# Kernel optimization log

Measured on AMD Instinct MI355X. Metric: run time of the kernel, lower is better.

Reference implementation:

```python
import jax, jax.numpy as jnp
import numpy as np

N = 50000      # nodes
E = 800000     # edges (avg degree 16)
CIN = 64       # in_channels
COUT = 128     # hidden_channels (block out_channels)
TC = 512       # time_channels = 4*hidden
H = 4          # attention heads
DH = COUT // H # head dim
G = 8          # group-norm groups
SLOPE = 0.01   # LeakyReLU default slope


def group_norm(x, w, b, groups=G, eps=1e-5):
    n, c = x.shape
    xg = x.reshape(n, groups, c // groups)
    mu = xg.mean(-1, keepdims=True)
    var = xg.var(-1, keepdims=True)
    xn = ((xg - mu) * jax.lax.rsqrt(var + eps)).reshape(n, c)
    return xn * w + b


def gcn_conv(x, W, b, row, col, ew, n):
    # GCNConv: add self loops (weight 1), symmetric normalization
    sl = jnp.arange(n)
    r = jnp.concatenate([row, sl])
    c = jnp.concatenate([col, sl])
    w2 = jnp.concatenate([ew, jnp.ones((n,), ew.dtype)])
    deg = jax.ops.segment_sum(w2, c, num_segments=n)
    dinv = jnp.where(deg > 0, jax.lax.rsqrt(deg), 0.0)
    norm = dinv[r] * w2 * dinv[c]            # [E+N]
    xw = x @ W                                # [N, Cout]
    out = jax.ops.segment_sum(norm[:, None] * xw[r], c, num_segments=n)
    return out + b


def gat_conv(x, Wa, a_src, a_dst, a_edge, ba, row, col, ew, n):
    # GAT-style attention conv; self-loop edge weight filled with max(edge_weight)
    sl = jnp.arange(n)
    fill = ew.max()
    r = jnp.concatenate([row, sl])
    c = jnp.concatenate([col, sl])
    w2 = jnp.concatenate([ew, jnp.full((n,), fill, ew.dtype)])
    h = (x @ Wa).reshape(n, H, DH)            # [N, H, DH]
    al_s = (h * a_src).sum(-1)                # [N, H]
    al_d = (h * a_dst).sum(-1)                # [N, H]
    logits = jax.nn.leaky_relu(al_s[r] + al_d[c] + a_edge * w2[:, None], 0.2)
    m = jax.ops.segment_max(logits, c, num_segments=n)
    e = jnp.exp(logits - m[c])
    s = jax.ops.segment_sum(e, c, num_segments=n)
    alpha = e / (s[c] + 1e-16)                # [E+N, H]
    out = jax.ops.segment_sum(alpha[:, :, None] * h[r], c, num_segments=n)
    return out.reshape(n, H * DH) + ba


def setup_inputs() -> dict:
    key = jax.random.key(0)
    ks = jax.random.split(key, 24)
    def w(k, shape, fan_in):
        return (jax.random.normal(k, shape, jnp.float32) / np.sqrt(fan_in)).astype(jnp.float32)
    inp = {
        "x": jax.random.normal(ks[0], (N, CIN), jnp.float32),
        "t": jax.random.normal(ks[1], (TC,), jnp.float32),
        "edge_index": jax.random.randint(ks[2], (2, E), 0, N, jnp.int32),
        "edge_weight": jax.random.uniform(ks[3], (E,), jnp.float32),
        # ResBlock norm/conv params
        "gn0_w": jnp.ones((CIN,), jnp.float32), "gn0_b": jnp.zeros((CIN,), jnp.float32),
        "W1": w(ks[4], (CIN, COUT), CIN), "b1": jnp.zeros((COUT,), jnp.float32),
        "gn1_w": jnp.ones((COUT,), jnp.float32), "gn1_b": jnp.zeros((COUT,), jnp.float32),
        "W2": w(ks[5], (COUT, COUT), COUT), "b2": jnp.zeros((COUT,), jnp.float32),
        "Wres": w(ks[6], (CIN, COUT), CIN),
        "te_w": w(ks[7], (TC, COUT), TC), "te_b": jnp.zeros((COUT,), jnp.float32),
        # AttnBlock params
        "gn2_w": jnp.ones((COUT,), jnp.float32), "gn2_b": jnp.zeros((COUT,), jnp.float32),
        "Wa": w(ks[8], (COUT, H * DH), COUT),
        "a_src": w(ks[9], (H, DH), DH), "a_dst": w(ks[10], (H, DH), DH),
        "a_edge": w(ks[11], (H,), 1), "ba": jnp.zeros((H * DH,), jnp.float32),
    }
    return inp


def reference(x, t, edge_index, edge_weight,
              gn0_w, gn0_b, W1, b1, gn1_w, gn1_b, W2, b2, Wres, te_w, te_b,
              gn2_w, gn2_b, Wa, a_src, a_dst, a_edge, ba):
    row, col = edge_index[0], edge_index[1]
    leaky = lambda z: jax.nn.leaky_relu(z, SLOPE)
    # ResBlock (n_layers=2)
    h = gcn_conv(leaky(group_norm(x, gn0_w, gn0_b)), W1, b1, row, col, edge_weight, N)
    tt = leaky(t) @ te_w + te_b               # time embed, broadcasts over nodes
    h = h + tt
    h = gcn_conv(leaky(group_norm(h, gn1_w, gn1_b)), W2, b2, row, col, edge_weight, N)
    h = h + x @ Wres                          # residual (Cin != Cout -> Linear)
    # AttnBlock (n_layers=1)
    a = leaky(group_norm(h, gn2_w, gn2_b))
    out = gat_conv(a, Wa, a_src, a_dst, a_edge, ba, row, col, edge_weight, N)
    return out
```

## Files before the change

kernel.cpp:

```cpp
#include <hip/hip_runtime.h>
#include <math.h>

#define ELLW 48
#define CH 4096
#define BCAP 8192

typedef __attribute__((ext_vector_type(8))) short frag_ab;
typedef __attribute__((ext_vector_type(4))) float frag_cd;

__device__ __forceinline__ float lk(float v, float s) { return v > 0.f ? v : v * s; }
__device__ __forceinline__ unsigned short f2b(float f) {
    unsigned u = __float_as_uint(f);
    return (unsigned short)((u + 0x7fffu + ((u >> 16) & 1u)) >> 16);
}
__device__ __forceinline__ float b2f(unsigned h) { return __uint_as_float(h << 16); }

template <int K>
__device__ __forceinline__ void repack1(const float* __restrict__ W,
                                        unsigned short* __restrict__ Wp, int i) {
    int k = i >> 7, nn = i & 127;
    int kc = k >> 5, quad = (k >> 3) & 3, j = k & 7;
    Wp[(((size_t)(kc * 4 + quad) * 128) + nn) * 8 + j] = f2b(W[i]);
}

__global__ __launch_bounds__(256) void k_bscatter(const int* __restrict__ row,
                                                  const int* __restrict__ col,
                                                  const float* __restrict__ ew,
                                                  int* __restrict__ cursor,
                                                  uint2* __restrict__ stage,
                                                  float* __restrict__ bmax,
                                                  int E, int NB, int gridE,
                                                  const float* __restrict__ t,
                                                  const float* __restrict__ te_w,
                                                  const float* __restrict__ te_b,
                                                  const float* __restrict__ b1,
                                                  float* __restrict__ tt,
                                                  const float* __restrict__ W1,
                                                  const float* __restrict__ W2,
                                                  const float* __restrict__ Wa,
                                                  const float* __restrict__ Wres,
                                                  unsigned short* W1p, unsigned short* W2p,
                                                  unsigned short* Wap, unsigned short* Wrp) {
    int tid = threadIdx.x;
    int blk = blockIdx.x;
    if (blk >= gridE) {
        if (blk == gridE) {
            if (tid < 128) {
                float s = te_b[tid] + b1[tid];
                for (int k = 0; k < 512; ++k) {
                    float tv = t[k]; tv = tv > 0.f ? tv : 0.01f * tv;
                    s = fmaf(tv, te_w[k * 128 + tid], s);
                }
                tt[tid] = s;
            }
        } else {
            int i = (blk - gridE - 1) * 256 + tid;
            if (i < 8192)        repack1<64>(W1, W1p, i);
            else if (i < 24576)  repack1<128>(W2, W2p, i - 8192);
            else if (i < 40960)  repack1<128>(Wa, Wap, i - 24576);
            else if (i < 49152)  repack1<64>(Wres, Wrp, i - 40960);
        }
        return;
    }
    __shared__ int lh[256];
    __shared__ int lbase[256];
    constexpr int PT = CH / 256;
    if (tid < NB) lh[tid] = 0;
    __syncthreads();
    int base = blk * CH;
    unsigned entry[PT]; int cc[PT]; int lpos[PT]; bool val[PT];
    float m = 0.f;
#pragma unroll
    for (int i = 0; i < PT; ++i) {
        int e = base + i * 256 + tid;
        val[i] = (e < E);
        entry[i] = 0; cc[i] = 0; lpos[i] = 0;
        if (val[i]) {
            int r = row[e], c = col[e];
            float w = ew[e];
            m = fmaxf(m, w);
            entry[i] = (unsigned)r | ((unsigned)f2b(w) << 16);
            cc[i] = c;
            lpos[i] = atomicAdd(&lh[c >> 8], 1);
        }
    }
    __syncthreads();
    if (tid < NB) lbase[tid] = lh[tid] ? atomicAdd(&cursor[tid], lh[tid]) : 0;
    __syncthreads();
#pragma unroll
    for (int i = 0; i < PT; ++i) {
        if (val[i]) {
            int b = cc[i] >> 8;
            int pos = lbase[b] + lpos[i];
            if (pos < BCAP)
                stage[(size_t)b * BCAP + pos] = make_uint2(entry[i], (unsigned)(cc[i] & 255));
        }
    }
    for (int o = 32; o; o >>= 1) m = fmaxf(m, __shfl_down(m, o, 64));
    __shared__ float sm[4];
    if ((tid & 63) == 0) sm[tid >> 6] = m;
    __syncthreads();
    if (tid == 0) bmax[blk] = fmaxf(fmaxf(sm[0], sm[1]), fmaxf(sm[2], sm[3]));
}

__global__ __launch_bounds__(256) void k_bbuild(const int* __restrict__ cursor,
                                                const uint2* __restrict__ stage,
                                                unsigned* __restrict__ ell,
                                                int* __restrict__ cnt,
                                                float* __restrict__ dinv,
                                                const float* __restrict__ bmax,
                                                float* __restrict__ fill, int n, int nbm) {
    __shared__ unsigned tile[256 * ELLW];
    __shared__ int lcnt[256];
    int tid = threadIdx.x;
    int bk = blockIdx.x;
    lcnt[tid] = 0;
    __syncthreads();
    if (bk == 0) {
        float m = 0.f;
        for (int i = tid; i < nbm; i += 256) m = fmaxf(m, bmax[i]);
        for (int o = 32; o; o >>= 1) m = fmaxf(m, __shfl_down(m, o, 64));
        __shared__ float sm[4];
        if ((tid & 63) == 0) sm[tid >> 6] = m;
        __syncthreads();
        if (tid == 0) *fill = fmaxf(fmaxf(sm[0], sm[1]), fmaxf(sm[2], sm[3]));
    }
    int bc = min(cursor[bk], BCAP);
    const uint2* sp = stage + (size_t)bk * BCAP;
    for (int i = tid; i < bc; i += 256) {
        uint2 p = sp[i];
        int c8 = p.y;
        int pos = atomicAdd(&lcnt[c8], 1);
        if (pos < ELLW) tile[c8 * ELLW + pos] = p.x;
    }
    __syncthreads();
    int node = bk * 256 + tid;
    if (node >= n) return;
    int c = min(lcnt[tid], ELLW);
    cnt[node] = c;
    float sw = 1.f;
    for (int j = 0; j < c; ++j) sw += b2f(tile[tid * ELLW + j] >> 16);
    dinv[node] = rsqrtf(sw);
    unsigned* dst = ell + (size_t)node * ELLW;
#pragma unroll
    for (int j = 0; j < ELLW / 4; ++j)
        *(uint4*)(dst + j * 4) = *(uint4*)(tile + tid * ELLW + j * 4);
}

__global__ __launch_bounds__(256) void k_mgemm1(const float* __restrict__ X,
                                                const float* __restrict__ gw,
                                                const float* __restrict__ gb,
                                                const unsigned short* __restrict__ Wp,
                                                unsigned short* __restrict__ OUTh,
                                                unsigned short* __restrict__ xh,
                                                const float* __restrict__ dinv, int n) {
    int tid = threadIdx.x;
    int wave = tid >> 6, lane = tid & 63;
    int quad = lane >> 4, l16 = lane & 15;
    int rbase = blockIdx.x * 64 + wave * 16;
    int arow = rbase + l16; if (arow >= n) arow = n - 1;
    frag_ab afrag[2];
    const float* xr = X + (size_t)arow * 64 + quad * 8;
#pragma unroll
    for (int kc = 0; kc < 2; ++kc) {
        float4 u0 = *(const float4*)(xr + kc * 32);
        float4 u1 = *(const float4*)(xr + kc * 32 + 4);
        float v[8] = {u0.x, u0.y, u0.z, u0.w, u1.x, u1.y, u1.z, u1.w};
        float s = 0.f, sq = 0.f;
#pragma unroll
        for (int j = 0; j < 8; ++j) { s += v[j]; sq = fmaf(v[j], v[j], sq); }
        float mu = s * 0.125f;
        float var = sq * 0.125f - mu * mu;
        float rstd = rsqrtf(var + 1e-5f);
        const float* wj = gw + kc * 32 + quad * 8;
        const float* bj = gb + kc * 32 + quad * 8;
        unsigned pk[4], pr[4];
#pragma unroll
        for (int j = 0; j < 8; j += 2) {
            float y0 = lk((v[j + 0] - mu) * rstd * wj[j + 0] + bj[j + 0], 0.01f);
            float y1 = lk((v[j + 1] - mu) * rstd * wj[j + 1] + bj[j + 1], 0.01f);
            pk[j / 2] = (unsigned)f2b(y0) | ((unsigned)f2b(y1) << 16);
            pr[j / 2] = (unsigned)f2b(v[j]) | ((unsigned)f2b(v[j + 1]) << 16);
        }
        afrag[kc] = *(frag_ab*)pk;
        *(uint4*)(xh + (size_t)arow * 64 + kc * 32 + quad * 8) = *(uint4*)pr;
    }
    frag_cd acc[8];
#pragma unroll
    for (int t = 0; t < 8; ++t) acc[t] = (frag_cd){0.f, 0.f, 0.f, 0.f};
#pragma unroll
    for (int kc = 0; kc < 2; ++kc) {
        const unsigned short* bp = Wp + ((size_t)(kc * 4 + quad) * 128 + l16) * 8;
#pragma unroll
        for (int t = 0; t < 8; ++t) {
            frag_ab b = *(const frag_ab*)(bp + (size_t)t * 128);
            acc[t] = __builtin_amdgcn_mfma_f32_16x16x32_bf16(afrag[kc], b, acc[t], 0, 0, 0);
        }
    }
#pragma unroll
    for (int reg = 0; reg < 4; ++reg) {
        int r = rbase + quad * 4 + reg;
        if (r >= n) continue;
        float sc = dinv[r];
#pragma unroll
        for (int t = 0; t < 8; ++t)
            OUTh[(size_t)r * 128 + t * 16 + l16] = f2b(sc * acc[t][reg]);
    }
}

__global__ __launch_bounds__(256) void k_mgemm2(const unsigned short* __restrict__ X1,
                                                const unsigned short* __restrict__ W2p,
                                                const unsigned short* __restrict__ X2,
                                                const unsigned short* __restrict__ Wrp,
                                                unsigned short* __restrict__ OUTh,
                                                float* __restrict__ C2,
                                                const float* __restrict__ bias,
                                                const float* __restrict__ dinv, int n) {
    int tid = threadIdx.x;
    int wave = tid >> 6, lane = tid & 63;
    int quad = lane >> 4, l16 = lane & 15;
    int rbase = blockIdx.x * 64 + wave * 16;
    int arow = rbase + l16; if (arow >= n) arow = n - 1;
    frag_cd acc1[8], acc2[8];
#pragma unroll
    for (int t = 0; t < 8; ++t) {
        acc1[t] = (frag_cd){0.f, 0.f, 0.f, 0.f};
        acc2[t] = (frag_cd){0.f, 0.f, 0.f, 0.f};
    }
    const unsigned short* ap1 = X1 + (size_t)arow * 128 + quad * 8;
#pragma unroll
    for (int kc = 0; kc < 4; ++kc) {
        frag_ab a = *(const frag_ab*)(ap1 + kc * 32);
        const unsigned short* bp = W2p + ((size_t)(kc * 4 + quad) * 128 + l16) * 8;
#pragma unroll
        for (int t = 0; t < 8; ++t) {
            frag_ab b = *(const frag_ab*)(bp + (size_t)t * 128);
            acc1[t] = __builtin_amdgcn_mfma_f32_16x16x32_bf16(a, b, acc1[t], 0, 0, 0);
        }
    }
    const unsigned short* ap2 = X2 + (size_t)arow * 64 + quad * 8;
#pragma unroll
    for (int kc = 0; kc < 2; ++kc) {
        frag_ab a = *(const frag_ab*)(ap2 + kc * 32);
        const unsigned short* bp = Wrp + ((size_t)(kc * 4 + quad) * 128 + l16) * 8;
#pragma unroll
        for (int t = 0; t < 8; ++t) {
            frag_ab b = *(const frag_ab*)(bp + (size_t)t * 128);
            acc2[t] = __builtin_amdgcn_mfma_f32_16x16x32_bf16(a, b, acc2[t], 0, 0, 0);
        }
    }
#pragma unroll
    for (int reg = 0; reg < 4; ++reg) {
        int r = rbase + quad * 4 + reg;
        if (r >= n) continue;
        float sc = dinv[r];
#pragma unroll
        for (int t = 0; t < 8; ++t) {
            int c = t * 16 + l16;
            size_t o = (size_t)r * 128 + c;
            OUTh[o] = f2b(sc * acc1[t][reg]);
            C2[o] = bias[c] + acc2[t][reg];
        }
    }
}

__global__ __launch_bounds__(256) void k_mgemmA(const unsigned short* __restrict__ Xh,
                                                const unsigned short* __restrict__ Wp,
                                                unsigned short* __restrict__ OUTh,
                                                const float* __restrict__ a_src,
                                                const float* __restrict__ a_dst,
                                                float* __restrict__ als,
                                                float* __restrict__ ald, int n) {
    int tid = threadIdx.x;
    int wave = tid >> 6, lane = tid & 63;
    int quad = lane >> 4, l16 = lane & 15;
    int rbase = blockIdx.x * 64 + wave * 16;
    int arow = rbase + l16; if (arow >= n) arow = n - 1;
    frag_cd acc[8];
#pragma unroll
    for (int t = 0; t < 8; ++t) acc[t] = (frag_cd){0.f, 0.f, 0.f, 0.f};
    const unsigned short* ap = Xh + (size_t)arow * 128 + quad * 8;
#pragma unroll
    for (int kc = 0; kc < 4; ++kc) {
        frag_ab a = *(const frag_ab*)(ap + kc * 32);
        const unsigned short* bp = Wp + ((size_t)(kc * 4 + quad) * 128 + l16) * 8;
#pragma unroll
        for (int t = 0; t < 8; ++t) {
            frag_ab b = *(const frag_ab*)(bp + (size_t)t * 128);
            acc[t] = __builtin_amdgcn_mfma_f32_16x16x32_bf16(a, b, acc[t], 0, 0, 0);
        }
    }
#pragma unroll
    for (int reg = 0; reg < 4; ++reg) {
        int r = rbase + quad * 4 + reg;
        if (r >= n) continue;
#pragma unroll
        for (int t = 0; t < 8; ++t)
            OUTh[(size_t)r * 128 + t * 16 + l16] = f2b(acc[t][reg]);
    }
    float ps[4][4], pd[4][4];
#pragma unroll
    for (int hd = 0; hd < 4; ++hd) {
        float slo = a_src[hd * 32 + l16], shi = a_src[hd * 32 + 16 + l16];
        float dlo = a_dst[hd * 32 + l16], dhi = a_dst[hd * 32 + 16 + l16];
#pragma unroll
        for (int reg = 0; reg < 4; ++reg) {
            ps[reg][hd] = fmaf(acc[2 * hd][reg], slo, acc[2 * hd + 1][reg] * shi);
            pd[reg][hd] = fmaf(acc[2 * hd][reg], dlo, acc[2 * hd + 1][reg] * dhi);
        }
    }
#pragma unroll
    for (int m = 1; m < 16; m <<= 1) {
#pragma unroll
        for (int reg = 0; reg < 4; ++reg)
#pragma unroll
            for (int hd = 0; hd < 4; ++hd) {
                ps[reg][hd] += __shfl_xor(ps[reg][hd], m, 64);
                pd[reg][hd] += __shfl_xor(pd[reg][hd], m, 64);
            }
    }
    if (l16 == 0) {
#pragma unroll
        for (int reg = 0; reg < 4; ++reg) {
            int r = rbase + quad * 4 + reg;
            if (r >= n) continue;
#pragma unroll
            for (int hd = 0; hd < 4; ++hd) {
                als[r * 4 + hd] = ps[reg][hd];
                ald[r * 4 + hd] = pd[reg][hd];
            }
        }
    }
}

template <int BASEVEC>
__global__ __launch_bounds__(256) void k_gather_gn(const int* __restrict__ cnt,
                                                   const unsigned* __restrict__ ell,
                                                   const float* __restrict__ dinv,
                                                   const unsigned short* __restrict__ Bh,
                                                   const float* __restrict__ basevec,
                                                   const float* __restrict__ basebuf,
                                                   const float* __restrict__ gw,
                                                   const float* __restrict__ gb,
                                                   unsigned short* __restrict__ outh, int n) {
    int gid = blockIdx.x * 256 + threadIdx.x;
    int node = gid >> 5, q = gid & 31;
    if (node >= n) return;
    int s = node * ELLW;
    int e2 = s + min(cnt[node], ELLW);
    float a0 = 0.f, a1 = 0.f, a2 = 0.f, a3 = 0.f;
    int j = s;
    for (; j + 8 <= e2; j += 8) {
        uint4 pa = *(const uint4*)(ell + j);
        uint4 pb = *(const uint4*)(ell + j + 4);
        unsigned pe[8] = {pa.x, pa.y, pa.z, pa.w, pb.x, pb.y, pb.z, pb.w};
        uint2 v[8];
#pragma unroll
        for (int k = 0; k < 8; ++k)
            v[k] = *(const uint2*)(Bh + (size_t)(pe[k] & 0xffffu) * 128 + q * 4);
#pragma unroll
        for (int k = 0; k < 8; ++k) {
            float w = b2f(pe[k] >> 16);
            a0 = fmaf(w, b2f(v[k].x & 0xffffu), a0);
            a1 = fmaf(w, b2f(v[k].x >> 16), a1);
            a2 = fmaf(w, b2f(v[k].y & 0xffffu), a2);
            a3 = fmaf(w, b2f(v[k].y >> 16), a3);
        }
    }
    if (j + 4 <= e2) {
        uint4 pa = *(const uint4*)(ell + j);
        unsigned pe[4] = {pa.x, pa.y, pa.z, pa.w};
        uint2 v[4];
#pragma unroll
        for (int k = 0; k < 4; ++k)
            v[k] = *(const uint2*)(Bh + (size_t)(pe[k] & 0xffffu) * 128 + q * 4);
#pragma unroll
        for (int k = 0; k < 4; ++k) {
            float w = b2f(pe[k] >> 16);
            a0 = fmaf(w, b2f(v[k].x & 0xffffu), a0);
            a1 = fmaf(w, b2f(v[k].x >> 16), a1);
            a2 = fmaf(w, b2f(v[k].y & 0xffffu), a2);
            a3 = fmaf(w, b2f(v[k].y >> 16), a3);
        }
        j += 4;
    }
    for (; j < e2; ++j) {
        unsigned pe = ell[j];
        float nw = b2f(pe >> 16);
        uint2 hv = *(const uint2*)(Bh + (size_t)(pe & 0xffffu) * 128 + q * 4);
        a0 = fmaf(nw, b2f(hv.x & 0xffffu), a0);
        a1 = fmaf(nw, b2f(hv.x >> 16), a1);
        a2 = fmaf(nw, b2f(hv.y & 0xffffu), a2);
        a3 = fmaf(nw, b2f(hv.y >> 16), a3);
    }
    float dc = dinv[node];
    uint2 sv = *(const uint2*)(Bh + (size_t)node * 128 + q * 4);
    a0 = dc * (a0 + b2f(sv.x & 0xffffu));
    a1 = dc * (a1 + b2f(sv.x >> 16));
    a2 = dc * (a2 + b2f(sv.y & 0xffffu));
    a3 = dc * (a3 + b2f(sv.y >> 16));
    float h0, h1, h2, h3;
    if constexpr (BASEVEC) {
        float4 bb = *(const float4*)(basevec + q * 4);
        h0 = bb.x + a0; h1 = bb.y + a1; h2 = bb.z + a2; h3 = bb.w + a3;
    } else {
        float4 bb = *(const float4*)(basebuf + (size_t)node * 128 + q * 4);
        h0 = bb.x + a0; h1 = bb.y + a1; h2 = bb.z + a2; h3 = bb.w + a3;
    }
    float sum = (h0 + h1) + (h2 + h3);
    float sq = fmaf(h0, h0, fmaf(h1, h1, fmaf(h2, h2, h3 * h3)));
    sum += __shfl_xor(sum, 1, 64); sum += __shfl_xor(sum, 2, 64);
    sq  += __shfl_xor(sq, 1, 64);  sq  += __shfl_xor(sq, 2, 64);
    float mu = sum * (1.0f / 16.0f);
    float var = sq * (1.0f / 16.0f) - mu * mu;
    float rstd = rsqrtf(var + 1e-5f);
    float4 gwv = *(const float4*)(gw + q * 4);
    float4 gbv = *(const float4*)(gb + q * 4);
    float y0 = lk((h0 - mu) * rstd * gwv.x + gbv.x, 0.01f);
    float y1 = lk((h1 - mu) * rstd * gwv.y + gbv.y, 0.01f);
    float y2 = lk((h2 - mu) * rstd * gwv.z + gbv.z, 0.01f);
    float y3 = lk((h3 - mu) * rstd * gwv.w + gbv.w, 0.01f);
    uint2 o;
    o.x = (unsigned)f2b(y0) | ((unsigned)f2b(y1) << 16);
    o.y = (unsigned)f2b(y2) | ((unsigned)f2b(y3) << 16);
    *(uint2*)(outh + (size_t)node * 128 + q * 4) = o;
}

__global__ __launch_bounds__(256) void k_gat_gather(const int* __restrict__ cnt,
                                                    const unsigned* __restrict__ ell,
                                                    const float* __restrict__ als,
                                                    const float* __restrict__ ald,
                                                    const float* __restrict__ a_edge,
                                                    const float* __restrict__ fill,
                                                    const unsigned short* __restrict__ HAh,
                                                    const float* __restrict__ ba,
                                                    float* __restrict__ out, int n) {
    int gid = blockIdx.x * 256 + threadIdx.x;
    int node = gid >> 5, q = gid & 31, hd = q >> 3;
    if (node >= n) return;
    int s = node * ELLW;
    int e2 = s + min(cnt[node], ELLW);
    float ae = a_edge[hd];
    float aldc = ald[node * 4 + hd];
    float wself = *fill;
    float pself = __expf(lk(als[node * 4 + hd] + aldc + ae * wself, 0.2f));
    float den = pself;
    uint2 hv = *(const uint2*)(HAh + (size_t)node * 128 + q * 4);
    float a0 = pself * b2f(hv.x & 0xffffu), a1 = pself * b2f(hv.x >> 16);
    float a2 = pself * b2f(hv.y & 0xffffu), a3 = pself * b2f(hv.y >> 16);
    int j = s;
    for (; j + 8 <= e2; j += 8) {
        uint4 pa = *(const uint4*)(ell + j);
        uint4 pb = *(const uint4*)(ell + j + 4);
        unsigned pe[8] = {pa.x, pa.y, pa.z, pa.w, pb.x, pb.y, pb.z, pb.w};
        float sl[8]; uint2 v[8];
#pragma unroll
        for (int k = 0; k < 8; ++k) {
            int r = pe[k] & 0xffffu;
            sl[k] = als[r * 4 + hd];
            v[k] = *(const uint2*)(HAh + (size_t)r * 128 + q * 4);
        }
#pragma unroll
        for (int k = 0; k < 8; ++k) {
            float pev = __expf(lk(sl[k] + aldc + ae * b2f(pe[k] >> 16), 0.2f));
            den += pev;
            a0 = fmaf(pev, b2f(v[k].x & 0xffffu), a0);
            a1 = fmaf(pev, b2f(v[k].x >> 16), a1);
            a2 = fmaf(pev, b2f(v[k].y & 0xffffu), a2);
            a3 = fmaf(pev, b2f(v[k].y >> 16), a3);
        }
    }
    if (j + 4 <= e2) {
        uint4 pa = *(const uint4*)(ell + j);
        unsigned pe[4] = {pa.x, pa.y, pa.z, pa.w};
        float sl[4]; uint2 v[4];
#pragma unroll
        for (int k = 0; k < 4; ++k) {
            int r = pe[k] & 0xffffu;
            sl[k] = als[r * 4 + hd];
            v[k] = *(const uint2*)(HAh + (size_t)r * 128 + q * 4);
        }
#pragma unroll
        for (int k = 0; k < 4; ++k) {
            float pev = __expf(lk(sl[k] + aldc + ae * b2f(pe[k] >> 16), 0.2f));
            den += pev;
            a0 = fmaf(pev, b2f(v[k].x & 0xffffu), a0);
            a1 = fmaf(pev, b2f(v[k].x >> 16), a1);
            a2 = fmaf(pev, b2f(v[k].y & 0xffffu), a2);
            a3 = fmaf(pev, b2f(v[k].y >> 16), a3);
        }
        j += 4;
    }
    for (; j < e2; ++j) {
        unsigned pe = ell[j];
        int r = pe & 0xffffu;
        float pev = __expf(lk(als[r * 4 + hd] + aldc + ae * b2f(pe >> 16), 0.2f));
        den += pev;
        uint2 v = *(const uint2*)(HAh + (size_t)r * 128 + q * 4);
        a0 = fmaf(pev, b2f(v.x & 0xffffu), a0);
        a1 = fmaf(pev, b2f(v.x >> 16), a1);
        a2 = fmaf(pev, b2f(v.y & 0xffffu), a2);
        a3 = fmaf(pev, b2f(v.y >> 16), a3);
    }
    float inv = 1.0f / (den + 1e-16f);
    const float* bb = ba + q * 4;
    float4 o;
    o.x = bb[0] + a0 * inv; o.y = bb[1] + a1 * inv;
    o.z = bb[2] + a2 * inv; o.w = bb[3] + a3 * inv;
    *(float4*)&out[(size_t)node * 128 + q * 4] = o;
}

extern "C" void kernel_launch(void* const* d_in, const int* in_sizes, int n_in,
                              void* d_out, int out_size, void* d_ws, size_t ws_size,
                              hipStream_t stream) {
    const float* x     = (const float*)d_in[0];
    const float* t     = (const float*)d_in[1];
    const int*   eidx  = (const int*)d_in[2];
    const float* ew    = (const float*)d_in[3];
    const float* gn0_w = (const float*)d_in[4];
    const float* gn0_b = (const float*)d_in[5];
    const float* W1    = (const float*)d_in[6];
    const float* b1    = (const float*)d_in[7];
    const float* gn1_w = (const float*)d_in[8];
    const float* gn1_b = (const float*)d_in[9];
    const float* W2    = (const float*)d_in[10];
    const float* b2    = (const float*)d_in[11];
    const float* Wres  = (const float*)d_in[12];
    const float* te_w  = (const float*)d_in[13];
    const float* te_b  = (const float*)d_in[14];
    const float* gn2_w = (const float*)d_in[15];
    const float* gn2_b = (const float*)d_in[16];
    const float* Wa    = (const float*)d_in[17];
    const float* a_src = (const float*)d_in[18];
    const float* a_dst = (const float*)d_in[19];
    const float* a_edge= (const float*)d_in[20];
    const float* ba    = (const float*)d_in[21];

    int n = in_sizes[0] / 64;
    int E = in_sizes[3];
    const int* rowp = eidx;
    const int* colp = eidx + E;
    int NB = (n + 255) >> 8;

    auto cdiv = [](long long a, long long b) { return (int)((a + b - 1) / b); };
    int gridE = cdiv(E, CH);

    char* p = (char*)d_ws;
    float* fC = (float*)p;                 p += (size_t)n * 128 * 4;
    unsigned short* fDh = (unsigned short*)p; p += (size_t)n * 128 * 2;
    unsigned short* fBh = (unsigned short*)p; p += (size_t)n * 128 * 2;
    unsigned short* xh  = (unsigned short*)p; p += (size_t)n * 64 * 2;
    unsigned* ell = (unsigned*)p;          p += (size_t)n * ELLW * 4;
    uint2* stage = (uint2*)p;              p += (size_t)NB * BCAP * 8;
    unsigned short* W1p   = (unsigned short*)p; p += 64 * 128 * 2;
    unsigned short* W2p   = (unsigned short*)p; p += 128 * 128 * 2;
    unsigned short* Wap   = (unsigned short*)p; p += 128 * 128 * 2;
    unsigned short* Wresp = (unsigned short*)p; p += 64 * 128 * 2;
    float* dinv = (float*)p;               p += (size_t)n * 4;
    float* tt  = (float*)p;                p += 128 * 4;
    float* fill = (float*)p;               p += 16;
    float* als = (float*)p;                p += (size_t)4 * n * 4;
    float* ald = (float*)p;                p += (size_t)4 * n * 4;
    int* cnt    = (int*)p;                 p += (size_t)n * 4;
    int* cursor = (int*)p;                 p += 256 * 4;
    float* bmax = (float*)p;               p += 4096 * 4;
    float* out = (float*)d_out;

    hipMemsetAsync(cursor, 0, NB * 4, stream);
    k_bscatter<<<gridE + 1 + 192, 256, 0, stream>>>(rowp, colp, ew, cursor, stage, bmax,
                                                    E, NB, gridE,
                                                    t, te_w, te_b, b1, tt,
                                                    W1, W2, Wa, Wres, W1p, W2p, Wap, Wresp);
    k_bbuild<<<NB, 256, 0, stream>>>(cursor, stage, ell, cnt, dinv, bmax, fill, n, gridE);

    k_mgemm1<<<cdiv(n, 64), 256, 0, stream>>>(x, gn0_w, gn0_b, W1p, fBh, xh, dinv, n);
    k_gather_gn<1><<<cdiv(32LL * n, 256), 256, 0, stream>>>(cnt, ell, dinv, fBh, tt, nullptr,
                                                            gn1_w, gn1_b, fDh, n);

    k_mgemm2<<<cdiv(n, 64), 256, 0, stream>>>(fDh, W2p, xh, Wresp, fBh, fC, b2, dinv, n);
    k_gather_gn<0><<<cdiv(32LL * n, 256), 256, 0, stream>>>(cnt, ell, dinv, fBh, nullptr, fC,
                                                            gn2_w, gn2_b, fDh, n);

    k_mgemmA<<<cdiv(n, 64), 256, 0, stream>>>(fDh, Wap, fBh, a_src, a_dst, als, ald, n);
    k_gat_gather<<<cdiv(32LL * n, 256), 256, 0, stream>>>(cnt, ell, als, ald, a_edge, fill, fBh, ba, out, n);
}
```

Measured before the change: 293.9 us.

## Split gather edge lists across two half-waves and store residual buffer in bf16

Each node in the three gather kernels is now handled by 64 lanes instead of 32. The two halves each process half of the ELL edge list and combine their partial sums with a cross-half shuffle, and only the first half writes the output. The self-loop term in the GAT gather moves after the reduction so it is added only once. Separately, the residual buffer C is stored in bf16 instead of fp32, which halves its write and read traffic at some cost in precision. The goal is shorter per-thread dependency chains and more memory parallelism in the latency-bound gathers, at the cost of twice the threads and redundant group-norm work in the second half.

```diff
diff --git a/kernel.cpp b/kernel.cpp
--- a/kernel.cpp
+++ b/kernel.cpp
@@ -213,7 +213,7 @@
                                                 const unsigned short* __restrict__ X2,
                                                 const unsigned short* __restrict__ Wrp,
                                                 unsigned short* __restrict__ OUTh,
-                                                float* __restrict__ C2,
+                                                unsigned short* __restrict__ C2h,
                                                 const float* __restrict__ bias,
                                                 const float* __restrict__ dinv, int n) {
     int tid = threadIdx.x;
@@ -259,7 +259,7 @@
             int c = t * 16 + l16;
             size_t o = (size_t)r * 128 + c;
             OUTh[o] = f2b(sc * acc1[t][reg]);
-            C2[o] = bias[c] + acc2[t][reg];
+            C2h[o] = f2b(bias[c] + acc2[t][reg]);
         }
     }
 }
@@ -339,15 +339,18 @@
                                                    const float* __restrict__ dinv,
                                                    const unsigned short* __restrict__ Bh,
                                                    const float* __restrict__ basevec,
-                                                   const float* __restrict__ basebuf,
+                                                   const unsigned short* __restrict__ basebufh,
                                                    const float* __restrict__ gw,
                                                    const float* __restrict__ gb,
                                                    unsigned short* __restrict__ outh, int n) {
     int gid = blockIdx.x * 256 + threadIdx.x;
-    int node = gid >> 5, q = gid & 31;
+    int node = gid >> 6, q = gid & 31, half = (gid >> 5) & 1;
     if (node >= n) return;
-    int s = node * ELLW;
-    int e2 = s + min(cnt[node], ELLW);
+    int c = min(cnt[node], ELLW);
+    int mid = ((c + 4) >> 3) << 2;
+    int s0 = node * ELLW;
+    int s = half ? (s0 + mid) : s0;
+    int e2 = half ? (s0 + c) : (s0 + mid);
     float a0 = 0.f, a1 = 0.f, a2 = 0.f, a3 = 0.f;
     int j = s;
     for (; j + 8 <= e2; j += 8) {
@@ -393,6 +396,10 @@
         a2 = fmaf(nw, b2f(hv.y & 0xffffu), a2);
         a3 = fmaf(nw, b2f(hv.y >> 16), a3);
     }
+    a0 += __shfl_xor(a0, 32, 64);
+    a1 += __shfl_xor(a1, 32, 64);
+    a2 += __shfl_xor(a2, 32, 64);
+    a3 += __shfl_xor(a3, 32, 64);
     float dc = dinv[node];
     uint2 sv = *(const uint2*)(Bh + (size_t)node * 128 + q * 4);
     a0 = dc * (a0 + b2f(sv.x & 0xffffu));
@@ -404,8 +411,9 @@
         float4 bb = *(const float4*)(basevec + q * 4);
         h0 = bb.x + a0; h1 = bb.y + a1; h2 = bb.z + a2; h3 = bb.w + a3;
     } else {
-        float4 bb = *(const float4*)(basebuf + (size_t)node * 128 + q * 4);
-        h0 = bb.x + a0; h1 = bb.y + a1; h2 = bb.z + a2; h3 = bb.w + a3;
+        uint2 bb = *(const uint2*)(basebufh + (size_t)node * 128 + q * 4);
+        h0 = b2f(bb.x & 0xffffu) + a0; h1 = b2f(bb.x >> 16) + a1;
+        h2 = b2f(bb.y & 0xffffu) + a2; h3 = b2f(bb.y >> 16) + a3;
     }
     float sum = (h0 + h1) + (h2 + h3);
     float sq = fmaf(h0, h0, fmaf(h1, h1, fmaf(h2, h2, h3 * h3)));
@@ -420,10 +428,12 @@
     float y1 = lk((h1 - mu) * rstd * gwv.y + gbv.y, 0.01f);
     float y2 = lk((h2 - mu) * rstd * gwv.z + gbv.z, 0.01f);
     float y3 = lk((h3 - mu) * rstd * gwv.w + gbv.w, 0.01f);
-    uint2 o;
-    o.x = (unsigned)f2b(y0) | ((unsigned)f2b(y1) << 16);
-    o.y = (unsigned)f2b(y2) | ((unsigned)f2b(y3) << 16);
-    *(uint2*)(outh + (size_t)node * 128 + q * 4) = o;
+    if (half == 0) {
+        uint2 o;
+        o.x = (unsigned)f2b(y0) | ((unsigned)f2b(y1) << 16);
+        o.y = (unsigned)f2b(y2) | ((unsigned)f2b(y3) << 16);
+        *(uint2*)(outh + (size_t)node * 128 + q * 4) = o;
+    }
 }
 
 __global__ __launch_bounds__(256) void k_gat_gather(const int* __restrict__ cnt,
@@ -436,18 +446,18 @@
                                                     const float* __restrict__ ba,
                                                     float* __restrict__ out, int n) {
     int gid = blockIdx.x * 256 + threadIdx.x;
-    int node = gid >> 5, q = gid & 31, hd = q >> 3;
+    int node = gid >> 6, q = gid & 31, half = (gid >> 5) & 1;
+    int hd = q >> 3;
     if (node >= n) return;
-    int s = node * ELLW;
-    int e2 = s + min(cnt[node], ELLW);
+    int c = min(cnt[node], ELLW);
+    int mid = ((c + 4) >> 3) << 2;
+    int s0 = node * ELLW;
+    int s = half ? (s0 + mid) : s0;
+    int e2 = half ? (s0 + c) : (s0 + mid);
     float ae = a_edge[hd];
     float aldc = ald[node * 4 + hd];
-    float wself = *fill;
-    float pself = __expf(lk(als[node * 4 + hd] + aldc + ae * wself, 0.2f));
-    float den = pself;
-    uint2 hv = *(const uint2*)(HAh + (size_t)node * 128 + q * 4);
-    float a0 = pself * b2f(hv.x & 0xffffu), a1 = pself * b2f(hv.x >> 16);
-    float a2 = pself * b2f(hv.y & 0xffffu), a3 = pself * b2f(hv.y >> 16);
+    float den = 0.f;
+    float a0 = 0.f, a1 = 0.f, a2 = 0.f, a3 = 0.f;
     int j = s;
     for (; j + 8 <= e2; j += 8) {
         uint4 pa = *(const uint4*)(ell + j);
@@ -502,12 +512,27 @@
         a2 = fmaf(pev, b2f(v.y & 0xffffu), a2);
         a3 = fmaf(pev, b2f(v.y >> 16), a3);
     }
-    float inv = 1.0f / (den + 1e-16f);
-    const float* bb = ba + q * 4;
-    float4 o;
-    o.x = bb[0] + a0 * inv; o.y = bb[1] + a1 * inv;
-    o.z = bb[2] + a2 * inv; o.w = bb[3] + a3 * inv;
-    *(float4*)&out[(size_t)node * 128 + q * 4] = o;
+    a0 += __shfl_xor(a0, 32, 64);
+    a1 += __shfl_xor(a1, 32, 64);
+    a2 += __shfl_xor(a2, 32, 64);
+    a3 += __shfl_xor(a3, 32, 64);
+    den += __shfl_xor(den, 32, 64);
+    float wself = *fill;
+    float pself = __expf(lk(als[node * 4 + hd] + aldc + ae * wself, 0.2f));
+    uint2 hv = *(const uint2*)(HAh + (size_t)node * 128 + q * 4);
+    den += pself;
+    a0 = fmaf(pself, b2f(hv.x & 0xffffu), a0);
+    a1 = fmaf(pself, b2f(hv.x >> 16), a1);
+    a2 = fmaf(pself, b2f(hv.y & 0xffffu), a2);
+    a3 = fmaf(pself, b2f(hv.y >> 16), a3);
+    if (half == 0) {
+        float inv = 1.0f / (den + 1e-16f);
+        const float* bb = ba + q * 4;
+        float4 o;
+        o.x = bb[0] + a0 * inv; o.y = bb[1] + a1 * inv;
+        o.z = bb[2] + a2 * inv; o.w = bb[3] + a3 * inv;
+        *(float4*)&out[(size_t)node * 128 + q * 4] = o;
+    }
 }
 
 extern "C" void kernel_launch(void* const* d_in, const int* in_sizes, int n_in,
@@ -546,7 +571,7 @@
     int gridE = cdiv(E, CH);
 
     char* p = (char*)d_ws;
-    float* fC = (float*)p;                 p += (size_t)n * 128 * 4;
+    unsigned short* fCh = (unsigned short*)p; p += (size_t)n * 128 * 2;
     unsigned short* fDh = (unsigned short*)p; p += (size_t)n * 128 * 2;
     unsigned short* fBh = (unsigned short*)p; p += (size_t)n * 128 * 2;
     unsigned short* xh  = (unsigned short*)p; p += (size_t)n * 64 * 2;
@@ -574,13 +599,13 @@
     k_bbuild<<<NB, 256, 0, stream>>>(cursor, stage, ell, cnt, dinv, bmax, fill, n, gridE);
 
     k_mgemm1<<<cdiv(n, 64), 256, 0, stream>>>(x, gn0_w, gn0_b, W1p, fBh, xh, dinv, n);
-    k_gather_gn<1><<<cdiv(32LL * n, 256), 256, 0, stream>>>(cnt, ell, dinv, fBh, tt, nullptr,
+    k_gather_gn<1><<<cdiv(64LL * n, 256), 256, 0, stream>>>(cnt, ell, dinv, fBh, tt, nullptr,
                                                             gn1_w, gn1_b, fDh, n);
 
-    k_mgemm2<<<cdiv(n, 64), 256, 0, stream>>>(fDh, W2p, xh, Wresp, fBh, fC, b2, dinv, n);
-    k_gather_gn<0><<<cdiv(32LL * n, 256), 256, 0, stream>>>(cnt, ell, dinv, fBh, nullptr, fC,
+    k_mgemm2<<<cdiv(n, 64), 256, 0, stream>>>(fDh, W2p, xh, Wresp, fBh, fCh, b2, dinv, n);
+    k_gather_gn<0><<<cdiv(64LL * n, 256), 256, 0, stream>>>(cnt, ell, dinv, fBh, nullptr, fCh,
                                                             gn2_w, gn2_b, fDh, n);
 
     k_mgemmA<<<cdiv(n, 64), 256, 0, stream>>>(fDh, Wap, fBh, a_src, a_dst, als, ald, n);
-    k_gat_gather<<<cdiv(32LL * n, 256), 256, 0, stream>>>(cnt, ell, als, ald, a_edge, fill, fBh, ba, out, n);
-}
+    k_gat_gather<<<cdiv(64LL * n, 256), 256, 0, stream>>>(cnt, ell, als, ald, a_edge, fill, fBh, ba, out, n);
+}
```

Measured after the change: 317.0 us. 1.08x slower.
